# Optimization experiments

Hardware: AMD Instinct MI355X
Metric: run time of the kernel (lower is better)

The kernel has to match this reference:

```python
import jax, jax.numpy as jnp
import numpy as np

N, K, G, E, OUT = 50000, 32, 512, 400000, 8
EPS = 1e-8


def setup_inputs() -> dict:
    key = jax.random.key(0)
    ks = jax.random.split(key, 9)
    X = jax.random.uniform(ks[0], (N, G), dtype=jnp.float32)          # counts-like, non-negative
    Mu = jax.random.uniform(ks[1], (K, G), dtype=jnp.float32)
    Var = jax.random.uniform(ks[2], (K, G), dtype=jnp.float32) + 0.5  # keep variances bounded away from 0
    edge_index = jax.random.randint(ks[3], (2, E), 0, N)
    # learned parameters
    W = jax.random.normal(ks[4], (N, K), dtype=jnp.float32) * 0.1     # module inits zeros; small randn for non-trivial grads
    S = jnp.ones((N, 1), jnp.float32)
    glorot = float(np.sqrt(6.0 / (G + OUT)))
    Wl = jax.random.uniform(ks[5], (G, OUT), jnp.float32, -glorot, glorot)
    bl = jnp.zeros((OUT,), jnp.float32)
    Wr = jax.random.uniform(ks[6], (G, OUT), jnp.float32, -glorot, glorot)
    br = jnp.zeros((OUT,), jnp.float32)
    att = jax.random.normal(ks[7], (OUT,), jnp.float32) * 0.3
    return dict(X=X, Mu=Mu, Var=Var, W=W, S=S, Wl=Wl, bl=bl, Wr=Wr, br=br, att=att, edge_index=edge_index)


def reference(X, Mu, Var, W, S, Wl, bl, Wr, br, att, edge_index):
    P = jax.nn.softmax(W, axis=1)                                     # [N,K]

    # Gaussian NLL term: F[n,k] = -0.5 * sum_g (X[n,g] - Mu[k,g]*S[n])^2 / Var[k,g]
    # expanded into three GEMM-shaped contractions to avoid the [N,K,G] intermediate
    inv_var = 1.0 / Var                                               # [K,G]
    q1 = (X * X) @ inv_var.T                                          # [N,K]
    q2 = X @ (Mu * inv_var).T                                         # [N,K]
    q3 = jnp.sum(Mu * Mu * inv_var, axis=1)                           # [K]
    s = S[:, 0]                                                       # [N]
    Fmat = -0.5 * (q1 - 2.0 * s[:, None] * q2 + (s * s)[:, None] * q3[None, :])
    ll_prot = jnp.sum(P * Fmat) / X.shape[0]

    # GATv2 attention (heads=1, out=8, no self loops): only alpha is consumed downstream
    src, dst = edge_index[0], edge_index[1]
    xl = X @ Wl + bl                                                  # source transform [N,8]
    xr = X @ Wr + br                                                  # target transform [N,8]
    e = jax.nn.leaky_relu(xl[src] + xr[dst], 0.2) @ att               # [E]
    # segment softmax over edges grouped by destination node
    m = jax.lax.stop_gradient(jax.ops.segment_max(e, dst, num_segments=N))
    ex = jnp.exp(e - m[dst])
    denom = jax.ops.segment_sum(ex, dst, num_segments=N)
    alpha = ex / denom[dst]                                           # [E]

    ce_space = -jnp.sum(P[src] * alpha[:, None] * jnp.log(P[dst] + EPS)) / X.shape[0]
    return ll_prot, ce_space, P
```

## Files before the change

kernel.cpp:

```cpp
#include <hip/hip_runtime.h>
#include <hip/hip_bf16.h>
#include <math.h>

#define N_NODES 50000
#define K_COMP  32
#define G_DIM   512
#define E_EDGES 400000
#define OUT_DIM 8
#define EPSV    1e-8f

#define NPB 16
#define NB_NODE (N_NODES / NPB)
#define NB_E1   ((E_EDGES / 2 + 255) / 256)
#define NB_CE   ((E_EDGES / 2 + 255) / 256)

typedef __attribute__((ext_vector_type(8))) short short8;
typedef __attribute__((ext_vector_type(8))) unsigned short ushort8;
typedef __attribute__((ext_vector_type(4))) unsigned short ushort4v;
typedef __attribute__((ext_vector_type(4))) float f32x4;

static const size_t OFF_T     = 0;
static const size_t OFF_Q3    = OFF_T + 80 * 512;
static const size_t OFF_XL    = OFF_Q3 + 64;
static const size_t OFF_XR    = OFF_XL + (size_t)N_NODES * 8;
static const size_t OFF_PC    = OFF_XR + (size_t)N_NODES * 8;
static const size_t OFF_LOGP  = OFF_PC + (size_t)N_NODES * 32;
static const size_t OFF_EX    = OFF_LOGP + (size_t)N_NODES * 32;
static const size_t OFF_DENOM = OFF_EX + E_EDGES;
static const size_t OFF_PLL   = OFF_DENOM + N_NODES;
static const size_t OFF_PCE   = OFF_PLL + 4096;

__device__ __forceinline__ unsigned short f2bf(float f) {
    __hip_bfloat16 h = __float2bfloat16(f);
    return *(unsigned short*)&h;
}
__device__ __forceinline__ float bf2f(unsigned short u) {
    unsigned v = ((unsigned)u) << 16;
    return __uint_as_float(v);
}

__global__ __launch_bounds__(256)
void prep_kernel(const float* __restrict__ Var, const float* __restrict__ Mu,
                 const float* __restrict__ Wl, const float* __restrict__ Wr,
                 unsigned short* __restrict__ Tb, float* __restrict__ denom,
                 float* __restrict__ q3) {
    int idx = blockIdx.x * 256 + threadIdx.x;
    if (idx < 80 * 512) {
        int r = idx >> 9;
        int g = idx & 511;
        float v;
        if (r < 32)      v = 1.0f / Var[r * 512 + g];
        else if (r < 64) { int k = r - 32; v = Mu[k * 512 + g] / Var[k * 512 + g]; }
        else if (r < 72) { int o = r - 64; v = Wl[g * 8 + o]; }
        else             { int o = r - 72; v = Wr[g * 8 + o]; }
        int dest = ((g >> 5) * 5 + (r >> 4)) * 512 + (r & 15) * 32 + (((g & 31) >> 3) << 3) + (g & 7);
        Tb[dest] = f2bf(v);
    }
    if (idx < N_NODES) denom[idx] = 0.0f;

    if (blockIdx.x < 32) {
        int k = blockIdx.x;
        int t = threadIdx.x;
        float s = 0.0f;
        for (int g = t; g < 512; g += 256) {
            float mu = Mu[k * 512 + g];
            s += mu * mu / Var[k * 512 + g];
        }
        for (int off = 32; off; off >>= 1) s += __shfl_down(s, off);
        __shared__ float sQ[4];
        if ((t & 63) == 0) sQ[t >> 6] = s;
        __syncthreads();
        if (t == 0) q3[k] = sQ[0] + sQ[1] + sQ[2] + sQ[3];
    }
}

__global__ __launch_bounds__(128, 5)
void node_kernel(const float* __restrict__ X, const float* __restrict__ W,
                 const float* __restrict__ S, const float* __restrict__ bl,
                 const float* __restrict__ br, const unsigned short* __restrict__ Tb,
                 const float* __restrict__ q3, float* __restrict__ outP,
                 unsigned short* __restrict__ Pcb, unsigned short* __restrict__ logPb,
                 float* __restrict__ xl, float* __restrict__ xr,
                 float* __restrict__ pll) {
    __shared__ float sAccH[2][NPB][81];
    __shared__ float sLL[2];

    const int t = threadIdx.x;
    const int lane = t & 63;
    const int wv = t >> 6;
    const int col = lane & 15;
    const int kg  = lane >> 4;

    const int node = blockIdx.x * NPB + col;
    const float* xrow = X + (size_t)node * 512 + wv * 256 + kg * 8;

    f32x4 acc[5];
#pragma unroll
    for (int i = 0; i < 5; ++i) acc[i] = (f32x4){0.f, 0.f, 0.f, 0.f};

    float4 v0 = *(const float4*)(xrow);
    float4 v1 = *(const float4*)(xrow + 4);

#pragma unroll
    for (int gc = 0; gc < 256; gc += 32) {
        float4 n0v, n1v;
        if (gc + 32 < 256) {
            n0v = *(const float4*)(xrow + gc + 32);
            n1v = *(const float4*)(xrow + gc + 36);
        }
        const unsigned short* bbase =
            Tb + (size_t)(wv * 8 + (gc >> 5)) * 5 * 512 + col * 32 + kg * 8;
        short8 b0 = *(const short8*)(bbase);
        short8 b1 = *(const short8*)(bbase + 512);
        short8 b2 = *(const short8*)(bbase + 1024);
        short8 b3 = *(const short8*)(bbase + 1536);
        short8 b4 = *(const short8*)(bbase + 2048);

        short8 ax, ax2;
        ax[0] = (short)f2bf(v0.x); ax[1] = (short)f2bf(v0.y);
        ax[2] = (short)f2bf(v0.z); ax[3] = (short)f2bf(v0.w);
        ax[4] = (short)f2bf(v1.x); ax[5] = (short)f2bf(v1.y);
        ax[6] = (short)f2bf(v1.z); ax[7] = (short)f2bf(v1.w);
        ax2[0] = (short)f2bf(v0.x * v0.x); ax2[1] = (short)f2bf(v0.y * v0.y);
        ax2[2] = (short)f2bf(v0.z * v0.z); ax2[3] = (short)f2bf(v0.w * v0.w);
        ax2[4] = (short)f2bf(v1.x * v1.x); ax2[5] = (short)f2bf(v1.y * v1.y);
        ax2[6] = (short)f2bf(v1.z * v1.z); ax2[7] = (short)f2bf(v1.w * v1.w);

        acc[0] = __builtin_amdgcn_mfma_f32_16x16x32_bf16(ax2, b0, acc[0], 0, 0, 0);
        acc[1] = __builtin_amdgcn_mfma_f32_16x16x32_bf16(ax2, b1, acc[1], 0, 0, 0);
        acc[2] = __builtin_amdgcn_mfma_f32_16x16x32_bf16(ax,  b2, acc[2], 0, 0, 0);
        acc[3] = __builtin_amdgcn_mfma_f32_16x16x32_bf16(ax,  b3, acc[3], 0, 0, 0);
        acc[4] = __builtin_amdgcn_mfma_f32_16x16x32_bf16(ax,  b4, acc[4], 0, 0, 0);

        v0 = n0v; v1 = n1v;
    }

#pragma unroll
    for (int tile = 0; tile < 5; ++tile)
#pragma unroll
        for (int r = 0; r < 4; ++r)
            sAccH[wv][kg * 4 + r][tile * 16 + col] = acc[tile][r];
    __syncthreads();

    const int nn = t >> 3;
    const int j = t & 7;
    const int n = blockIdx.x * NPB + nn;

    float sv = S[n];
    float sv2 = sv * sv;
    float4 wv4 = *(const float4*)(W + (size_t)n * 32 + j * 4);
    float w[4] = {wv4.x, wv4.y, wv4.z, wv4.w};
    float wm = fmaxf(fmaxf(w[0], w[1]), fmaxf(w[2], w[3]));
    wm = fmaxf(wm, __shfl_xor(wm, 1));
    wm = fmaxf(wm, __shfl_xor(wm, 2));
    wm = fmaxf(wm, __shfl_xor(wm, 4));
    float p[4], ps = 0.0f;
#pragma unroll
    for (int i = 0; i < 4; ++i) { p[i] = expf(w[i] - wm); ps += p[i]; }
    ps += __shfl_xor(ps, 1);
    ps += __shfl_xor(ps, 2);
    ps += __shfl_xor(ps, 4);
    float inv = 1.0f / ps;

    float pv[4];
    ushort4v pb, lb;
    float ll = 0.0f;
#pragma unroll
    for (int i = 0; i < 4; ++i) {
        int k = j * 4 + i;
        float P_ = p[i] * inv;
        pv[i] = P_;
        pb[i] = f2bf(P_);
        lb[i] = f2bf(logf(P_ + EPSV));
        float q1k = sAccH[0][nn][k] + sAccH[1][nn][k];
        float q2k = sAccH[0][nn][32 + k] + sAccH[1][nn][32 + k];
        float f = -0.5f * (q1k - 2.0f * sv * q2k + sv2 * q3[k]);
        ll = fmaf(P_, f, ll);
    }
    ll += __shfl_xor(ll, 1);
    ll += __shfl_xor(ll, 2);
    ll += __shfl_xor(ll, 4);
    float llacc = (j == 0) ? ll : 0.0f;

    size_t base = (size_t)n * 32 + j * 4;
    float2* op = (float2*)(outP + base);
    op[0] = make_float2(pv[0], pv[1]);
    op[1] = make_float2(pv[2], pv[3]);
    *(ushort4v*)&Pcb[base] = pb;
    *(ushort4v*)&logPb[base] = lb;

    float xlv = (sAccH[0][nn][64 + j] + sAccH[1][nn][64 + j]) + bl[j];
    float xrv = (sAccH[0][nn][72 + j] + sAccH[1][nn][72 + j]) + br[j];
    xl[(size_t)n * 8 + j] = xlv;
    xr[(size_t)n * 8 + j] = xrv;

    for (int off = 32; off; off >>= 1) llacc += __shfl_down(llacc, off);
    if ((t & 63) == 0) sLL[wv] = llacc;
    __syncthreads();
    if (t == 0) pll[blockIdx.x] = sLL[0] + sLL[1];
}

__global__ __launch_bounds__(256)
void edge1_kernel(const int* __restrict__ ei, const float* __restrict__ xl,
                  const float* __restrict__ xr, const float* __restrict__ att,
                  float* __restrict__ ex, float* __restrict__ denom) {
    const int base = (blockIdx.x * 256 + threadIdx.x) * 2;
    if (base >= E_EDGES) return;
    int2 ss = *(const int2*)&ei[base];
    int2 dd = *(const int2*)&ei[E_EDGES + base];
    const float4* a0p = (const float4*)(xl + (size_t)ss.x * 8);
    const float4* b0p = (const float4*)(xr + (size_t)dd.x * 8);
    const float4* a1p = (const float4*)(xl + (size_t)ss.y * 8);
    const float4* b1p = (const float4*)(xr + (size_t)dd.y * 8);
    float4 a00 = a0p[0], a01 = a0p[1];
    float4 b00 = b0p[0], b01 = b0p[1];
    float4 a10 = a1p[0], a11 = a1p[1];
    float4 b10 = b1p[0], b11 = b1p[1];
    const float4* atp = (const float4*)att;
    float4 t0 = atp[0], t1 = atp[1];
    float at[8] = {t0.x, t0.y, t0.z, t0.w, t1.x, t1.y, t1.z, t1.w};
    float h0[8] = {a00.x + b00.x, a00.y + b00.y, a00.z + b00.z, a00.w + b00.w,
                   a01.x + b01.x, a01.y + b01.y, a01.z + b01.z, a01.w + b01.w};
    float h1[8] = {a10.x + b10.x, a10.y + b10.y, a10.z + b10.z, a10.w + b10.w,
                   a11.x + b11.x, a11.y + b11.y, a11.z + b11.z, a11.w + b11.w};
    float e0 = 0.0f, e1 = 0.0f;
#pragma unroll
    for (int q = 0; q < 8; ++q) {
        float v0 = h0[q]; v0 = v0 > 0.0f ? v0 : 0.2f * v0;
        float v1 = h1[q]; v1 = v1 > 0.0f ? v1 : 0.2f * v1;
        e0 = fmaf(v0, at[q], e0);
        e1 = fmaf(v1, at[q], e1);
    }
    float x0 = expf(e0), x1 = expf(e1);
    *(float2*)&ex[base] = make_float2(x0, x1);
    atomicAdd(denom + dd.x, x0);
    atomicAdd(denom + dd.y, x1);
}

__global__ __launch_bounds__(256, 4)
void edge2_kernel(const int* __restrict__ ei, const float* __restrict__ ex,
                  const float* __restrict__ denom,
                  const unsigned short* __restrict__ Pcb,
                  const unsigned short* __restrict__ logPb,
                  float* __restrict__ pce) {
    const int t = threadIdx.x;
    const int base = (blockIdx.x * 256 + t) * 2;
    float ce = 0.0f;
    if (base < E_EDGES) {
        int2 ss = *(const int2*)&ei[base];
        int2 dd = *(const int2*)&ei[E_EDGES + base];
        float2 xv = *(const float2*)&ex[base];
        const ushort8* p0p = (const ushort8*)&Pcb[(size_t)ss.x * 32];
        const ushort8* l0p = (const ushort8*)&logPb[(size_t)dd.x * 32];
        const ushort8* p1p = (const ushort8*)&Pcb[(size_t)ss.y * 32];
        const ushort8* l1p = (const ushort8*)&logPb[(size_t)dd.y * 32];
        ushort8 p0a = p0p[0], p0b = p0p[1], p0c = p0p[2], p0d = p0p[3];
        ushort8 l0a = l0p[0], l0b = l0p[1], l0c = l0p[2], l0d = l0p[3];
        ushort8 p1a = p1p[0], p1b = p1p[1], p1c = p1p[2], p1d = p1p[3];
        ushort8 l1a = l1p[0], l1b = l1p[1], l1c = l1p[2], l1d = l1p[3];
        float den0 = denom[dd.x];
        float den1 = denom[dd.y];
        float dot0 = 0.0f, dot1 = 0.0f;
#pragma unroll
        for (int r = 0; r < 8; ++r) {
            dot0 = fmaf(bf2f(p0a[r]), bf2f(l0a[r]), dot0);
            dot0 = fmaf(bf2f(p0b[r]), bf2f(l0b[r]), dot0);
            dot0 = fmaf(bf2f(p0c[r]), bf2f(l0c[r]), dot0);
            dot0 = fmaf(bf2f(p0d[r]), bf2f(l0d[r]), dot0);
            dot1 = fmaf(bf2f(p1a[r]), bf2f(l1a[r]), dot1);
            dot1 = fmaf(bf2f(p1b[r]), bf2f(l1b[r]), dot1);
            dot1 = fmaf(bf2f(p1c[r]), bf2f(l1c[r]), dot1);
            dot1 = fmaf(bf2f(p1d[r]), bf2f(l1d[r]), dot1);
        }
        ce = (xv.x / den0) * dot0 + (xv.y / den1) * dot1;
    }
    for (int off = 32; off; off >>= 1) ce += __shfl_down(ce, off);
    __shared__ float sC[4];
    if ((t & 63) == 0) sC[t >> 6] = ce;
    __syncthreads();
    if (t == 0) pce[blockIdx.x] = sC[0] + sC[1] + sC[2] + sC[3];
}

__global__ __launch_bounds__(256)
void finalize_kernel(const float* __restrict__ pll, const float* __restrict__ pce,
                     float* __restrict__ out) {
    const int t = threadIdx.x;
    float a = 0.0f, b = 0.0f;
    for (int i = t; i < NB_NODE; i += 256) a += pll[i];
    for (int i = t; i < NB_CE; i += 256) b += pce[i];
    for (int off = 32; off; off >>= 1) {
        a += __shfl_down(a, off);
        b += __shfl_down(b, off);
    }
    __shared__ float sA[4], sB[4];
    if ((t & 63) == 0) { sA[t >> 6] = a; sB[t >> 6] = b; }
    __syncthreads();
    if (t == 0) {
        float ll = sA[0] + sA[1] + sA[2] + sA[3];
        float ce = sB[0] + sB[1] + sB[2] + sB[3];
        out[0] = ll / (float)N_NODES;
        out[1] = -ce / (float)N_NODES;
    }
}

extern "C" void kernel_launch(void* const* d_in, const int* in_sizes, int n_in,
                              void* d_out, int out_size, void* d_ws, size_t ws_size,
                              hipStream_t stream) {
    const float* X   = (const float*)d_in[0];
    const float* Mu  = (const float*)d_in[1];
    const float* Var = (const float*)d_in[2];
    const float* W   = (const float*)d_in[3];
    const float* S   = (const float*)d_in[4];
    const float* Wl  = (const float*)d_in[5];
    const float* bl  = (const float*)d_in[6];
    const float* Wr  = (const float*)d_in[7];
    const float* br  = (const float*)d_in[8];
    const float* att = (const float*)d_in[9];
    const int*   ei  = (const int*)d_in[10];
    float* out = (float*)d_out;
    float* ws  = (float*)d_ws;

    unsigned short* Tb    = (unsigned short*)(ws + OFF_T);
    float*          q3    = ws + OFF_Q3;
    float*          xl    = ws + OFF_XL;
    float*          xr    = ws + OFF_XR;
    unsigned short* Pcb   = (unsigned short*)(ws + OFF_PC);
    unsigned short* logPb = (unsigned short*)(ws + OFF_LOGP);
    float*          ex    = ws + OFF_EX;
    float*          denom = ws + OFF_DENOM;
    float*          pll   = ws + OFF_PLL;
    float*          pce   = ws + OFF_PCE;

    prep_kernel<<<(N_NODES + 255) / 256, 256, 0, stream>>>(Var, Mu, Wl, Wr, Tb, denom, q3);
    node_kernel<<<NB_NODE, 128, 0, stream>>>(X, W, S, bl, br, Tb, q3,
                                             out + 2, Pcb, logPb, xl, xr, pll);
    edge1_kernel<<<NB_E1, 256, 0, stream>>>(ei, xl, xr, att, ex, denom);
    edge2_kernel<<<NB_CE, 256, 0, stream>>>(ei, ex, denom, Pcb, logPb, pce);
    finalize_kernel<<<1, 256, 0, stream>>>(pll, pce, out);
}
```

Measured before the change: 92.15 us.

## Fuse P·logP edge dot into attention kernel, shrink second pass to scalar gather

Moves the per-edge dot product of source P with destination log P into the first edge kernel, which now handles one edge per thread and stores x*dot per edge. The second edge pass then reads only one float per edge plus the denominator, instead of gathering two 64-byte bf16 rows per edge. This cuts redundant index and row gathers across the two edge passes. It also switches softmax exp/log in the node and edge kernels to fast intrinsics, and adds an occupancy bound on the first edge kernel. The trade-off is heavier register use and gather load in the first kernel.

```diff
diff --git a/kernel.cpp b/kernel.cpp
--- a/kernel.cpp
+++ b/kernel.cpp
@@ -11,7 +11,7 @@
 
 #define NPB 16
 #define NB_NODE (N_NODES / NPB)
-#define NB_E1   ((E_EDGES / 2 + 255) / 256)
+#define NB_E1   ((E_EDGES + 255) / 256)
 #define NB_CE   ((E_EDGES / 2 + 255) / 256)
 
 typedef __attribute__((ext_vector_type(8))) short short8;
@@ -25,8 +25,8 @@
 static const size_t OFF_XR    = OFF_XL + (size_t)N_NODES * 8;
 static const size_t OFF_PC    = OFF_XR + (size_t)N_NODES * 8;
 static const size_t OFF_LOGP  = OFF_PC + (size_t)N_NODES * 32;
-static const size_t OFF_EX    = OFF_LOGP + (size_t)N_NODES * 32;
-static const size_t OFF_DENOM = OFF_EX + E_EDGES;
+static const size_t OFF_CON   = OFF_LOGP + (size_t)N_NODES * 32;
+static const size_t OFF_DENOM = OFF_CON + E_EDGES;
 static const size_t OFF_PLL   = OFF_DENOM + N_NODES;
 static const size_t OFF_PCE   = OFF_PLL + 4096;
 
@@ -156,7 +156,7 @@
     wm = fmaxf(wm, __shfl_xor(wm, 4));
     float p[4], ps = 0.0f;
 #pragma unroll
-    for (int i = 0; i < 4; ++i) { p[i] = expf(w[i] - wm); ps += p[i]; }
+    for (int i = 0; i < 4; ++i) { p[i] = __expf(w[i] - wm); ps += p[i]; }
     ps += __shfl_xor(ps, 1);
     ps += __shfl_xor(ps, 2);
     ps += __shfl_xor(ps, 4);
@@ -171,7 +171,7 @@
         float P_ = p[i] * inv;
         pv[i] = P_;
         pb[i] = f2bf(P_);
-        lb[i] = f2bf(logf(P_ + EPSV));
+        lb[i] = f2bf(__logf(P_ + EPSV));
         float q1k = sAccH[0][nn][k] + sAccH[1][nn][k];
         float q2k = sAccH[0][nn][32 + k] + sAccH[1][nn][32 + k];
         float f = -0.5f * (q1k - 2.0f * sv * q2k + sv2 * q3[k]);
@@ -200,79 +200,62 @@
     if (t == 0) pll[blockIdx.x] = sLL[0] + sLL[1];
 }
 
-__global__ __launch_bounds__(256)
+__global__ __launch_bounds__(256, 4)
 void edge1_kernel(const int* __restrict__ ei, const float* __restrict__ xl,
                   const float* __restrict__ xr, const float* __restrict__ att,
-                  float* __restrict__ ex, float* __restrict__ denom) {
-    const int base = (blockIdx.x * 256 + threadIdx.x) * 2;
-    if (base >= E_EDGES) return;
-    int2 ss = *(const int2*)&ei[base];
-    int2 dd = *(const int2*)&ei[E_EDGES + base];
-    const float4* a0p = (const float4*)(xl + (size_t)ss.x * 8);
-    const float4* b0p = (const float4*)(xr + (size_t)dd.x * 8);
-    const float4* a1p = (const float4*)(xl + (size_t)ss.y * 8);
-    const float4* b1p = (const float4*)(xr + (size_t)dd.y * 8);
-    float4 a00 = a0p[0], a01 = a0p[1];
-    float4 b00 = b0p[0], b01 = b0p[1];
-    float4 a10 = a1p[0], a11 = a1p[1];
-    float4 b10 = b1p[0], b11 = b1p[1];
+                  const unsigned short* __restrict__ Pcb,
+                  const unsigned short* __restrict__ logPb,
+                  float* __restrict__ contrib, float* __restrict__ denom) {
+    int i = blockIdx.x * 256 + threadIdx.x;
+    if (i >= E_EDGES) return;
+    int s = ei[i];
+    int d = ei[E_EDGES + i];
+    const float4* ap = (const float4*)(xl + (size_t)s * 8);
+    const float4* bp = (const float4*)(xr + (size_t)d * 8);
+    const ushort8* pp = (const ushort8*)&Pcb[(size_t)s * 32];
+    const ushort8* lp = (const ushort8*)&logPb[(size_t)d * 32];
+    float4 a0 = ap[0], a1 = ap[1];
+    float4 b0 = bp[0], b1 = bp[1];
+    ushort8 pa = pp[0], pb_ = pp[1], pc = pp[2], pd = pp[3];
+    ushort8 la = lp[0], lb_ = lp[1], lc = lp[2], ld = lp[3];
     const float4* atp = (const float4*)att;
     float4 t0 = atp[0], t1 = atp[1];
     float at[8] = {t0.x, t0.y, t0.z, t0.w, t1.x, t1.y, t1.z, t1.w};
-    float h0[8] = {a00.x + b00.x, a00.y + b00.y, a00.z + b00.z, a00.w + b00.w,
-                   a01.x + b01.x, a01.y + b01.y, a01.z + b01.z, a01.w + b01.w};
-    float h1[8] = {a10.x + b10.x, a10.y + b10.y, a10.z + b10.z, a10.w + b10.w,
-                   a11.x + b11.x, a11.y + b11.y, a11.z + b11.z, a11.w + b11.w};
-    float e0 = 0.0f, e1 = 0.0f;
+    float h[8] = {a0.x + b0.x, a0.y + b0.y, a0.z + b0.z, a0.w + b0.w,
+                  a1.x + b1.x, a1.y + b1.y, a1.z + b1.z, a1.w + b1.w};
+    float ev = 0.0f;
 #pragma unroll
     for (int q = 0; q < 8; ++q) {
-        float v0 = h0[q]; v0 = v0 > 0.0f ? v0 : 0.2f * v0;
-        float v1 = h1[q]; v1 = v1 > 0.0f ? v1 : 0.2f * v1;
-        e0 = fmaf(v0, at[q], e0);
-        e1 = fmaf(v1, at[q], e1);
-    }
-    float x0 = expf(e0), x1 = expf(e1);
-    *(float2*)&ex[base] = make_float2(x0, x1);
-    atomicAdd(denom + dd.x, x0);
-    atomicAdd(denom + dd.y, x1);
+        float hv = h[q];
+        hv = hv > 0.0f ? hv : 0.2f * hv;
+        ev = fmaf(hv, at[q], ev);
+    }
+    float x = __expf(ev);
+    atomicAdd(denom + d, x);
+
+    float dot = 0.0f;
+#pragma unroll
+    for (int r = 0; r < 8; ++r) {
+        dot = fmaf(bf2f(pa[r]),  bf2f(la[r]),  dot);
+        dot = fmaf(bf2f(pb_[r]), bf2f(lb_[r]), dot);
+        dot = fmaf(bf2f(pc[r]),  bf2f(lc[r]),  dot);
+        dot = fmaf(bf2f(pd[r]),  bf2f(ld[r]),  dot);
+    }
+    contrib[i] = x * dot;
 }
 
 __global__ __launch_bounds__(256, 4)
-void edge2_kernel(const int* __restrict__ ei, const float* __restrict__ ex,
-                  const float* __restrict__ denom,
-                  const unsigned short* __restrict__ Pcb,
-                  const unsigned short* __restrict__ logPb,
-                  float* __restrict__ pce) {
+void edge2_kernel(const int* __restrict__ ei, const float* __restrict__ contrib,
+                  const float* __restrict__ denom, float* __restrict__ pce) {
     const int t = threadIdx.x;
     const int base = (blockIdx.x * 256 + t) * 2;
     float ce = 0.0f;
     if (base < E_EDGES) {
-        int2 ss = *(const int2*)&ei[base];
         int2 dd = *(const int2*)&ei[E_EDGES + base];
-        float2 xv = *(const float2*)&ex[base];
-        const ushort8* p0p = (const ushort8*)&Pcb[(size_t)ss.x * 32];
-        const ushort8* l0p = (const ushort8*)&logPb[(size_t)dd.x * 32];
-        const ushort8* p1p = (const ushort8*)&Pcb[(size_t)ss.y * 32];
-        const ushort8* l1p = (const ushort8*)&logPb[(size_t)dd.y * 32];
-        ushort8 p0a = p0p[0], p0b = p0p[1], p0c = p0p[2], p0d = p0p[3];
-        ushort8 l0a = l0p[0], l0b = l0p[1], l0c = l0p[2], l0d = l0p[3];
-        ushort8 p1a = p1p[0], p1b = p1p[1], p1c = p1p[2], p1d = p1p[3];
-        ushort8 l1a = l1p[0], l1b = l1p[1], l1c = l1p[2], l1d = l1p[3];
+        float2 cv = *(const float2*)&contrib[base];
         float den0 = denom[dd.x];
         float den1 = denom[dd.y];
-        float dot0 = 0.0f, dot1 = 0.0f;
-#pragma unroll
-        for (int r = 0; r < 8; ++r) {
-            dot0 = fmaf(bf2f(p0a[r]), bf2f(l0a[r]), dot0);
-            dot0 = fmaf(bf2f(p0b[r]), bf2f(l0b[r]), dot0);
-            dot0 = fmaf(bf2f(p0c[r]), bf2f(l0c[r]), dot0);
-            dot0 = fmaf(bf2f(p0d[r]), bf2f(l0d[r]), dot0);
-            dot1 = fmaf(bf2f(p1a[r]), bf2f(l1a[r]), dot1);
-            dot1 = fmaf(bf2f(p1b[r]), bf2f(l1b[r]), dot1);
-            dot1 = fmaf(bf2f(p1c[r]), bf2f(l1c[r]), dot1);
-            dot1 = fmaf(bf2f(p1d[r]), bf2f(l1d[r]), dot1);
-        }
-        ce = (xv.x / den0) * dot0 + (xv.y / den1) * dot1;
+        ce = cv.x / den0 + cv.y / den1;
     }
     for (int off = 32; off; off >>= 1) ce += __shfl_down(ce, off);
     __shared__ float sC[4];
@@ -320,21 +303,21 @@
     float* out = (float*)d_out;
     float* ws  = (float*)d_ws;
 
-    unsigned short* Tb    = (unsigned short*)(ws + OFF_T);
-    float*          q3    = ws + OFF_Q3;
-    float*          xl    = ws + OFF_XL;
-    float*          xr    = ws + OFF_XR;
-    unsigned short* Pcb   = (unsigned short*)(ws + OFF_PC);
-    unsigned short* logPb = (unsigned short*)(ws + OFF_LOGP);
-    float*          ex    = ws + OFF_EX;
-    float*          denom = ws + OFF_DENOM;
-    float*          pll   = ws + OFF_PLL;
-    float*          pce   = ws + OFF_PCE;
+    unsigned short* Tb      = (unsigned short*)(ws + OFF_T);
+    float*          q3      = ws + OFF_Q3;
+    float*          xl      = ws + OFF_XL;
+    float*          xr      = ws + OFF_XR;
+    unsigned short* Pcb     = (unsigned short*)(ws + OFF_PC);
+    unsigned short* logPb   = (unsigned short*)(ws + OFF_LOGP);
+    float*          contrib = ws + OFF_CON;
+    float*          denom   = ws + OFF_DENOM;
+    float*          pll     = ws + OFF_PLL;
+    float*          pce     = ws + OFF_PCE;
 
     prep_kernel<<<(N_NODES + 255) / 256, 256, 0, stream>>>(Var, Mu, Wl, Wr, Tb, denom, q3);
     node_kernel<<<NB_NODE, 128, 0, stream>>>(X, W, S, bl, br, Tb, q3,
                                              out + 2, Pcb, logPb, xl, xr, pll);
-    edge1_kernel<<<NB_E1, 256, 0, stream>>>(ei, xl, xr, att, ex, denom);
-    edge2_kernel<<<NB_CE, 256, 0, stream>>>(ei, ex, denom, Pcb, logPb, pce);
+    edge1_kernel<<<NB_E1, 256, 0, stream>>>(ei, xl, xr, att, Pcb, logPb, contrib, denom);
+    edge2_kernel<<<NB_CE, 256, 0, stream>>>(ei, contrib, denom, pce);
     finalize_kernel<<<1, 256, 0, stream>>>(pll, pce, out);
 }
```

Result: faster. 80.94 us (-12.2%).
